# Performance work log

Measured on AMD Instinct MI355X. Metric: run time of the kernel, lower is better.

## Reference

```python
import jax, jax.numpy as jnp
import numpy as np

N_NODES = 50000
N_GRAPHS = 256
IN_DIM = 128
HID = 128
N_LAYERS = 3
N_EDGES = 800000


def setup_inputs() -> dict:
    key = jax.random.key(0)
    ks = jax.random.split(key, 16)
    x = jax.random.normal(ks[0], (N_NODES, IN_DIM), dtype=jnp.float32)
    edge_index = jax.random.randint(ks[1], (2, N_EDGES), 0, N_NODES, dtype=jnp.int64)
    batch = jnp.sort(jax.random.randint(ks[2], (N_NODES,), 0, N_GRAPHS, dtype=jnp.int64))
    inp = {"x": x, "edge_index": edge_index, "batch": batch}
    # SAGEConv params per PyG: lin_l (bias) applied to mean-aggregated neighbors,
    # lin_r (no bias) applied to the root node feature.
    dims = [(IN_DIM, HID)] + [(HID, HID)] * (N_LAYERS - 1)
    for i, (din, dout) in enumerate(dims):
        s = 1.0 / np.sqrt(din)
        inp[f"Wl{i}"] = jax.random.uniform(ks[3 + 3 * i], (din, dout), jnp.float32, -s, s)
        inp[f"bl{i}"] = jax.random.uniform(ks[4 + 3 * i], (dout,), jnp.float32, -s, s)
        inp[f"Wr{i}"] = jax.random.uniform(ks[5 + 3 * i], (din, dout), jnp.float32, -s, s)
    return inp


def _sage_conv(x, src, dst, Wl, bl, Wr):
    # mean aggregation of source-node messages into destination nodes
    msg = x[src]                                               # [E, d] gather
    agg = jax.ops.segment_sum(msg, dst, num_segments=N_NODES)  # [N, d] scatter-add
    deg = jax.ops.segment_sum(jnp.ones((src.shape[0], 1), x.dtype), dst,
                              num_segments=N_NODES)
    agg = agg / jnp.maximum(deg, 1.0)
    return agg @ Wl + bl + x @ Wr


def reference(x, edge_index, batch, Wl0, bl0, Wr0, Wl1, bl1, Wr1, Wl2, bl2, Wr2):
    src, dst = edge_index[0], edge_index[1]
    params = [(Wl0, bl0, Wr0), (Wl1, bl1, Wr1), (Wl2, bl2, Wr2)]
    h = x
    for Wl, bl, Wr in params:
        h = jax.nn.relu(_sage_conv(h, src, dst, Wl, bl, Wr))
        # dropout is a no-op in eval mode
    # meanmax readout over graph ids
    cnt = jax.ops.segment_sum(jnp.ones((h.shape[0], 1), h.dtype), batch,
                              num_segments=N_GRAPHS)
    g_mean = jax.ops.segment_sum(h, batch, num_segments=N_GRAPHS) / jnp.maximum(cnt, 1.0)
    g_max = jax.ops.segment_max(h, batch, num_segments=N_GRAPHS)
    g_max = jnp.where(jnp.isfinite(g_max), g_max, 0.0)  # empty graphs -> 0
    return jnp.concatenate([g_mean, g_max], axis=-1)    # [G, 2*HID]
```

## Files before the change

kernel.cpp:

```cpp
#include <hip/hip_runtime.h>
#include <hip/hip_bf16.h>
#include <stdint.h>

#define N_NODES  50000
#define N_GRAPHS 256
#define DIM      128
#define N_EDGES  800000
#define K2       256
#define N_STRIPS (N_NODES / 16)
#define PAD_CAP  64

typedef __attribute__((ext_vector_type(8))) short  short8;
typedef __attribute__((ext_vector_type(4))) float  floatx4;
typedef __attribute__((ext_vector_type(4))) int    intx4;

__device__ __forceinline__ ushort f2bf(float f) {
    union { float f; uint32_t u; } c; c.f = f;
    uint32_t u = c.u;
    return (ushort)((u + 0x7fffu + ((u >> 16) & 1u)) >> 16);
}

#define MB_CONV 6250
#define MB_PREPW (MB_CONV + 384)
#define MB_GB   (MB_PREPW + 196)
#define MB_CNT  (MB_GB + 196)
#define MB_OUT  (MB_CNT + 256)
__global__ __launch_bounds__(256) void k_misc(const float* __restrict__ x, ushort* __restrict__ xb,
                                              const float* __restrict__ Wl0, const float* __restrict__ Wr0,
                                              const float* __restrict__ Wl1, const float* __restrict__ Wr1,
                                              const float* __restrict__ Wl2, const float* __restrict__ Wr2,
                                              ushort* __restrict__ Wt,
                                              const int* __restrict__ batch,
                                              int* __restrict__ gstart, int* __restrict__ gend,
                                              int* __restrict__ cnt, float* __restrict__ out) {
    int b = blockIdx.x, t = threadIdx.x;
    if (b < MB_CONV) {
        int i = b * 256 + t;
        float4 v = ((const float4*)x)[i];
        uint32_t lo = (uint32_t)f2bf(v.x) | ((uint32_t)f2bf(v.y) << 16);
        uint32_t hi = (uint32_t)f2bf(v.z) | ((uint32_t)f2bf(v.w) << 16);
        ((uint2*)xb)[i] = make_uint2(lo, hi);
    } else if (b < MB_PREPW) {
        int i = (b - MB_CONV) * 256 + t;
        int layer = i / (DIM * K2);
        int j = i % (DIM * K2);
        int n = j / K2, k = j % K2;
        const float* Wl = (layer == 0) ? Wl0 : (layer == 1) ? Wl1 : Wl2;
        const float* Wr = (layer == 0) ? Wr0 : (layer == 1) ? Wr1 : Wr2;
        float v = (k < DIM) ? Wl[k * DIM + n] : Wr[(k - DIM) * DIM + n];
        Wt[i] = f2bf(v);
    } else if (b < MB_GB) {
        int i = (b - MB_PREPW) * 256 + t;
        if (i < N_NODES) {
            int g = batch[i];
            if (i == 0) gstart[g] = 0;
            int gn = (i + 1 < N_NODES) ? batch[i + 1] : -1;
            if (gn != g) {
                gend[g] = i + 1;
                if (gn >= 0) gstart[gn] = i + 1;
            }
        }
    } else if (b < MB_CNT) {
        int i = (b - MB_GB) * 256 + t;
        if (i < N_NODES) cnt[i] = 0;
    } else {
        int i = (b - MB_CNT) * 256 + t;
        if (i < N_GRAPHS * 2 * DIM) out[i] = 0.f;
    }
}

__global__ __launch_bounds__(256) void k_build_direct(const int* __restrict__ src,
                                                      const int* __restrict__ dst,
                                                      int* __restrict__ cnt,
                                                      int* __restrict__ padded) {
    int i = blockIdx.x * 256 + threadIdx.x;
    if (i < N_EDGES) {
        int d = dst[i], s = src[i];
        int p = atomicAdd(&cnt[d], 1);
        if (p < PAD_CAP) padded[(size_t)d * PAD_CAP + p] = s;
    }
}

template <int MODE>
__global__ __launch_bounds__(256) void k_layer(const ushort* __restrict__ h_in,
                                               int* __restrict__ padded,
                                               const int* __restrict__ cnt,
                                               const ushort* __restrict__ Wt,
                                               const float* __restrict__ bias,
                                               ushort* __restrict__ out_bf,
                                               const int* __restrict__ batch,
                                               float* __restrict__ gout) {
    __shared__ ushort sAgg[16 * DIM];
    __shared__ int    sIdx[16 * PAD_CAP];
    __shared__ int    sCnt[16];
    __shared__ int    sChl[4][17];
    __shared__ int    sNch[4];
    __shared__ int    sGb[(MODE == 2) ? 16 : 1];
    __shared__ float  hTile[(MODE == 2) ? 16 * DIM : 1];

    int t    = threadIdx.x;
    int wid  = t >> 6;
    int lane = t & 63;
    int r0   = blockIdx.x * 16;
    const uint32_t* hw = (const uint32_t*)h_in;

    ((intx4*)sIdx)[t] = __builtin_nontemporal_load(
        ((const intx4*)(padded + (size_t)r0 * PAD_CAP)) + t);
    if (t < 16) sCnt[t] = cnt[r0 + t];
    if (MODE == 2 && t >= 16 && t < 32) sGb[t - 16] = batch[r0 + t - 16];
    __syncthreads();

    if (MODE == 0) {
        #pragma unroll
        for (int q = 0; q < 4; ++q) {
            int nl  = wid * 4 + q;
            int m   = min(sCnt[nl], PAD_CAP);
            int* lst = sIdx + nl * PAD_CAP;
            int v = (lane < m) ? lst[lane] : 0x7fffffff;
            #pragma unroll
            for (int k = 2; k <= 64; k <<= 1) {
                #pragma unroll
                for (int j = k >> 1; j > 0; j >>= 1) {
                    int other  = __shfl_xor(v, j, 64);
                    bool down  = (lane & k) != 0;
                    bool lower = (lane & j) == 0;
                    v = (lower ^ down) ? min(v, other) : max(v, other);
                }
            }
            if (lane < m) {
                lst[lane] = v;
                __builtin_nontemporal_store(v,
                    &padded[(size_t)(r0 + nl) * PAD_CAP + lane]);
            }
        }
    }

    if (lane == 0) {
        int n = 0;
        #pragma unroll
        for (int q = 0; q < 4; ++q) {
            int m = min(sCnt[wid * 4 + q], PAD_CAP);
            for (int e0 = 0; e0 < m; e0 += 16)
                sChl[wid][n++] = q | (e0 << 8);
        }
        sNch[wid] = n;
    }
    #pragma unroll
    for (int q = 0; q < 4; ++q) {
        int node = wid * 4 + q;
        if (sCnt[node] == 0) ((uint32_t*)(sAgg + node * DIM))[lane] = 0u;
    }
    int nch = sNch[wid];

    float ax[4] = {0.f, 0.f, 0.f, 0.f};
    float ay[4] = {0.f, 0.f, 0.f, 0.f};
    uint32_t va[16], vb[16];

    auto issue = [&](int ci, uint32_t (&v)[16]) {
        int ch   = sChl[wid][ci];
        int q    = ch & 255, e0 = ch >> 8;
        int node = wid * 4 + q;
        int m    = min(sCnt[node], PAD_CAP);
        const int* lst = sIdx + node * PAD_CAP;
        #pragma unroll
        for (int k = 0; k < 16; ++k) {
            int ek = e0 + k;
            int id = lst[ek < m ? ek : m - 1];
            v[k] = hw[(size_t)id * 64 + lane];
        }
    };
    auto consume = [&](int ci, uint32_t (&v)[16], bool isLast) {
        int ch   = sChl[wid][ci];
        int q    = ch & 255, e0 = ch >> 8;
        int node = wid * 4 + q;
        int deg  = sCnt[node];
        int m    = min(deg, PAD_CAP);
        #pragma unroll
        for (int k = 0; k < 16; ++k) {
            uint32_t w = (e0 + k < m) ? v[k] : 0u;
            ax[k & 3] += __uint_as_float(w << 16);
            ay[k & 3] += __uint_as_float(w & 0xffff0000u);
        }
        bool lastOfNode = isLast || ((sChl[wid][ci + 1] & 255) != q);
        if (lastOfNode) {
            float axs = (ax[0] + ax[1]) + (ax[2] + ax[3]);
            float ays = (ay[0] + ay[1]) + (ay[2] + ay[3]);
            float inv = 1.0f / (float)(deg > 0 ? deg : 1);
            uint32_t o = (uint32_t)f2bf(axs * inv) | ((uint32_t)f2bf(ays * inv) << 16);
            ((uint32_t*)(sAgg + node * DIM))[lane] = o;
            #pragma unroll
            for (int j = 0; j < 4; ++j) { ax[j] = 0.f; ay[j] = 0.f; }
        }
    };

    if (nch > 0) {
        issue(0, va);
        int i = 0;
        while (true) {
            bool hasB = (i + 1) < nch;
            if (hasB) issue(i + 1, vb);
            consume(i, va, !hasB);
            if (!hasB) break;
            bool hasA = (i + 2) < nch;
            if (hasA) issue(i + 2, va);
            consume(i + 1, vb, !hasA);
            if (!hasA) break;
            i += 2;
        }
    }
    __syncthreads();

    int row  = lane & 15;
    int quad = lane >> 4;
    short8 a[8];
    const ushort* srow = sAgg + row * DIM + quad * 8;
    #pragma unroll
    for (int ks = 0; ks < 4; ++ks) a[ks] = *(const short8*)(srow + ks * 32);
    const ushort* hrow = h_in + (size_t)(r0 + row) * DIM + quad * 8;
    #pragma unroll
    for (int ks = 0; ks < 4; ++ks) a[4 + ks] = *(const short8*)(hrow + ks * 32);

    #pragma unroll
    for (int c = 0; c < 2; ++c) {
        int ct  = wid * 2 + c;
        int col = ct * 16 + row;
        const ushort* wrow = Wt + (size_t)col * K2 + quad * 8;
        floatx4 acc = {0.f, 0.f, 0.f, 0.f};
        #pragma unroll
        for (int ks = 0; ks < 8; ++ks) {
            short8 b = *(const short8*)(wrow + ks * 32);
            acc = __builtin_amdgcn_mfma_f32_16x16x32_bf16(a[ks], b, acc, 0, 0, 0);
        }
        float bv = bias[col];
        #pragma unroll
        for (int r = 0; r < 4; ++r) {
            int m = r0 + quad * 4 + r;
            float v = acc[r] + bv;
            v = v > 0.f ? v : 0.f;
            if (MODE < 2) __builtin_nontemporal_store(f2bf(v), &out_bf[(size_t)m * DIM + col]);
            else          hTile[(quad * 4 + r) * DIM + col] = v;
        }
    }

    if (MODE == 2) {
        __syncthreads();
        int d     = t & 127;
        bool doMax = t >= 128;
        float s = 0.f, mx = 0.f;
        int cur = sGb[0];
        #pragma unroll
        for (int m = 0; m < 16; ++m) {
            int g = sGb[m];
            if (g != cur) {
                if (doMax) atomicMax((int*)&gout[cur * 2 * DIM + DIM + d], __float_as_int(mx));
                else       atomicAdd(&gout[cur * 2 * DIM + d], s);
                cur = g; s = 0.f; mx = 0.f;
            }
            float v = hTile[m * DIM + d];
            s += v; mx = fmaxf(mx, v);
        }
        if (doMax) atomicMax((int*)&gout[cur * 2 * DIM + DIM + d], __float_as_int(mx));
        else       atomicAdd(&gout[cur * 2 * DIM + d], s);
    }
}

__global__ __launch_bounds__(256) void k_finalize(float* __restrict__ out,
                                                  const int* __restrict__ gstart,
                                                  const int* __restrict__ gend) {
    int i = blockIdx.x * 256 + threadIdx.x;
    if (i < N_GRAPHS * DIM) {
        int g = i / DIM, d = i % DIM;
        int c = gend[g] - gstart[g];
        out[g * 2 * DIM + d] /= (float)(c > 0 ? c : 1);
    }
}

extern "C" void kernel_launch(void* const* d_in, const int* in_sizes, int n_in,
                              void* d_out, int out_size, void* d_ws, size_t ws_size,
                              hipStream_t stream) {
    const float* x     = (const float*)d_in[0];
    const int*   ei    = (const int*)d_in[1];
    const int*   src   = ei;
    const int*   dst   = ei + N_EDGES;
    const int*   batch = (const int*)d_in[2];
    const float* Wl[3] = {(const float*)d_in[3], (const float*)d_in[6], (const float*)d_in[9]};
    const float* bl[3] = {(const float*)d_in[4], (const float*)d_in[7], (const float*)d_in[10]};
    const float* Wr[3] = {(const float*)d_in[5], (const float*)d_in[8], (const float*)d_in[11]};
    float* out = (float*)d_out;

    char* base = (char*)d_ws;
    size_t o = 0;
    auto alloc = [&](size_t b) -> char* {
        char* p = base + o;
        o = (o + b + 255) & ~(size_t)255;
        return p;
    };
    int*     gstart = (int*)alloc((size_t)N_GRAPHS * 4);
    int*     gend   = (int*)alloc((size_t)N_GRAPHS * 4);
    int*     cnt    = (int*)alloc((size_t)N_NODES * 4);
    int*     padded = (int*)alloc((size_t)N_NODES * PAD_CAP * 4);
    ushort*  xb     = (ushort*)alloc((size_t)N_NODES * DIM * 2);
    ushort*  ha     = (ushort*)alloc((size_t)N_NODES * DIM * 2);
    ushort*  hb     = (ushort*)alloc((size_t)N_NODES * DIM * 2);
    ushort*  Wt     = (ushort*)alloc((size_t)3 * DIM * K2 * 2);
    (void)ws_size; (void)n_in; (void)in_sizes; (void)out_size;

    k_misc<<<MB_OUT, 256, 0, stream>>>(x, xb, Wl[0], Wr[0], Wl[1], Wr[1], Wl[2], Wr[2],
                                       Wt, batch, gstart, gend, cnt, out);
    k_build_direct<<<(N_EDGES + 255) / 256, 256, 0, stream>>>(src, dst, cnt, padded);

    k_layer<0><<<N_STRIPS, 256, 0, stream>>>(xb, padded, cnt, Wt,                bl[0], ha, batch, out);
    k_layer<1><<<N_STRIPS, 256, 0, stream>>>(ha, padded, cnt, Wt + DIM * K2,     bl[1], hb, batch, out);
    k_layer<2><<<N_STRIPS, 256, 0, stream>>>(hb, padded, cnt, Wt + 2 * DIM * K2, bl[2], nullptr, batch, out);

    k_finalize<<<(N_GRAPHS * DIM + 255) / 256, 256, 0, stream>>>(out, gstart, gend);
}
```

Measured before the change: 327.4 us.

## Give each wave its own 16-node strip and drop block barriers in layer kernel

Each wavefront now handles a whole 16-node strip on its own: it loads the strip's neighbour lists, sorts and gathers them, and runs all 8 MFMA column tiles. Blocks therefore carry four independent strips and need no __syncthreads. The aggregation buffer reuses the index shared memory. The final-layer readout now reduces sum and max per graph segment with cross-lane shuffles and issues fewer atomics, instead of staging a shared tile. The edge-build scatter uses nontemporal stores. In exchange, each wave does more serial work and holds more registers, and the grid has a quarter as many blocks.

```diff
diff --git a/kernel.cpp b/kernel.cpp
--- a/kernel.cpp
+++ b/kernel.cpp
@@ -77,7 +77,7 @@
     if (i < N_EDGES) {
         int d = dst[i], s = src[i];
         int p = atomicAdd(&cnt[d], 1);
-        if (p < PAD_CAP) padded[(size_t)d * PAD_CAP + p] = s;
+        if (p < PAD_CAP) __builtin_nontemporal_store(s, &padded[(size_t)d * PAD_CAP + p]);
     }
 }
 
@@ -90,32 +90,32 @@
                                                ushort* __restrict__ out_bf,
                                                const int* __restrict__ batch,
                                                float* __restrict__ gout) {
-    __shared__ ushort sAgg[16 * DIM];
-    __shared__ int    sIdx[16 * PAD_CAP];
-    __shared__ int    sCnt[16];
-    __shared__ int    sChl[4][17];
-    __shared__ int    sNch[4];
-    __shared__ int    sGb[(MODE == 2) ? 16 : 1];
-    __shared__ float  hTile[(MODE == 2) ? 16 * DIM : 1];
-
-    int t    = threadIdx.x;
-    int wid  = t >> 6;
-    int lane = t & 63;
-    int r0   = blockIdx.x * 16;
+    __shared__ int sIA[4][16 * 64];
+    __shared__ int sCnt[4][16];
+    __shared__ int sChl[4][65];
+    __shared__ int sGb[4][16];
+
+    int t     = threadIdx.x;
+    int wid   = t >> 6;
+    int lane  = t & 63;
+    int strip = blockIdx.x * 4 + wid;
+    if (strip >= N_STRIPS) return;
+    int r0    = strip * 16;
+    int* sIdx = sIA[wid];
     const uint32_t* hw = (const uint32_t*)h_in;
 
-    ((intx4*)sIdx)[t] = __builtin_nontemporal_load(
-        ((const intx4*)(padded + (size_t)r0 * PAD_CAP)) + t);
-    if (t < 16) sCnt[t] = cnt[r0 + t];
-    if (MODE == 2 && t >= 16 && t < 32) sGb[t - 16] = batch[r0 + t - 16];
-    __syncthreads();
+    const intx4* gsrc = (const intx4*)(padded + (size_t)r0 * PAD_CAP);
+    #pragma unroll
+    for (int it = 0; it < 4; ++it)
+        ((intx4*)sIdx)[it * 64 + lane] = __builtin_nontemporal_load(gsrc + it * 64 + lane);
+    if (lane < 16) sCnt[wid][lane] = cnt[r0 + lane];
+    if (MODE == 2 && lane >= 16 && lane < 32) sGb[wid][lane - 16] = batch[r0 + lane - 16];
 
     if (MODE == 0) {
-        #pragma unroll
-        for (int q = 0; q < 4; ++q) {
-            int nl  = wid * 4 + q;
-            int m   = min(sCnt[nl], PAD_CAP);
-            int* lst = sIdx + nl * PAD_CAP;
+        #pragma unroll 1
+        for (int q = 0; q < 16; ++q) {
+            int m = min(sCnt[wid][q], PAD_CAP);
+            int* lst = sIdx + q * 64;
             int v = (lane < m) ? lst[lane] : 0x7fffffff;
             #pragma unroll
             for (int k = 2; k <= 64; k <<= 1) {
@@ -130,38 +130,35 @@
             if (lane < m) {
                 lst[lane] = v;
                 __builtin_nontemporal_store(v,
-                    &padded[(size_t)(r0 + nl) * PAD_CAP + lane]);
+                    &padded[(size_t)(r0 + q) * PAD_CAP + lane]);
             }
         }
     }
 
     if (lane == 0) {
         int n = 0;
-        #pragma unroll
-        for (int q = 0; q < 4; ++q) {
-            int m = min(sCnt[wid * 4 + q], PAD_CAP);
+        #pragma unroll 1
+        for (int q = 0; q < 16; ++q) {
+            int m = min(sCnt[wid][q], PAD_CAP);
             for (int e0 = 0; e0 < m; e0 += 16)
                 sChl[wid][n++] = q | (e0 << 8);
         }
-        sNch[wid] = n;
-    }
-    #pragma unroll
-    for (int q = 0; q < 4; ++q) {
-        int node = wid * 4 + q;
-        if (sCnt[node] == 0) ((uint32_t*)(sAgg + node * DIM))[lane] = 0u;
-    }
-    int nch = sNch[wid];
+        sChl[wid][64] = n;
+    }
+    #pragma unroll 1
+    for (int q = 0; q < 16; ++q)
+        if (sCnt[wid][q] == 0) ((uint32_t*)(sIdx + q * 64))[lane] = 0u;
+    int nch = sChl[wid][64];
 
     float ax[4] = {0.f, 0.f, 0.f, 0.f};
     float ay[4] = {0.f, 0.f, 0.f, 0.f};
     uint32_t va[16], vb[16];
 
     auto issue = [&](int ci, uint32_t (&v)[16]) {
-        int ch   = sChl[wid][ci];
-        int q    = ch & 255, e0 = ch >> 8;
-        int node = wid * 4 + q;
-        int m    = min(sCnt[node], PAD_CAP);
-        const int* lst = sIdx + node * PAD_CAP;
+        int ch = sChl[wid][ci];
+        int q  = ch & 255, e0 = ch >> 8;
+        int m  = min(sCnt[wid][q], PAD_CAP);
+        const int* lst = sIdx + q * 64;
         #pragma unroll
         for (int k = 0; k < 16; ++k) {
             int ek = e0 + k;
@@ -170,11 +167,10 @@
         }
     };
     auto consume = [&](int ci, uint32_t (&v)[16], bool isLast) {
-        int ch   = sChl[wid][ci];
-        int q    = ch & 255, e0 = ch >> 8;
-        int node = wid * 4 + q;
-        int deg  = sCnt[node];
-        int m    = min(deg, PAD_CAP);
+        int ch  = sChl[wid][ci];
+        int q   = ch & 255, e0 = ch >> 8;
+        int deg = sCnt[wid][q];
+        int m   = min(deg, PAD_CAP);
         #pragma unroll
         for (int k = 0; k < 16; ++k) {
             uint32_t w = (e0 + k < m) ? v[k] : 0u;
@@ -187,7 +183,7 @@
             float ays = (ay[0] + ay[1]) + (ay[2] + ay[3]);
             float inv = 1.0f / (float)(deg > 0 ? deg : 1);
             uint32_t o = (uint32_t)f2bf(axs * inv) | ((uint32_t)f2bf(ays * inv) << 16);
-            ((uint32_t*)(sAgg + node * DIM))[lane] = o;
+            ((uint32_t*)(sIdx + q * 64))[lane] = o;
             #pragma unroll
             for (int j = 0; j < 4; ++j) { ax[j] = 0.f; ay[j] = 0.f; }
         }
@@ -208,21 +204,19 @@
             i += 2;
         }
     }
-    __syncthreads();
 
     int row  = lane & 15;
     int quad = lane >> 4;
     short8 a[8];
-    const ushort* srow = sAgg + row * DIM + quad * 8;
+    const ushort* srow = (const ushort*)sIdx + row * 128 + quad * 8;
     #pragma unroll
     for (int ks = 0; ks < 4; ++ks) a[ks] = *(const short8*)(srow + ks * 32);
     const ushort* hrow = h_in + (size_t)(r0 + row) * DIM + quad * 8;
     #pragma unroll
     for (int ks = 0; ks < 4; ++ks) a[4 + ks] = *(const short8*)(hrow + ks * 32);
 
-    #pragma unroll
-    for (int c = 0; c < 2; ++c) {
-        int ct  = wid * 2 + c;
+    #pragma unroll 1
+    for (int ct = 0; ct < 8; ++ct) {
         int col = ct * 16 + row;
         const ushort* wrow = Wt + (size_t)col * K2 + quad * 8;
         floatx4 acc = {0.f, 0.f, 0.f, 0.f};
@@ -232,35 +226,42 @@
             acc = __builtin_amdgcn_mfma_f32_16x16x32_bf16(a[ks], b, acc, 0, 0, 0);
         }
         float bv = bias[col];
+        float v[4];
         #pragma unroll
         for (int r = 0; r < 4; ++r) {
-            int m = r0 + quad * 4 + r;
-            float v = acc[r] + bv;
-            v = v > 0.f ? v : 0.f;
-            if (MODE < 2) __builtin_nontemporal_store(f2bf(v), &out_bf[(size_t)m * DIM + col]);
-            else          hTile[(quad * 4 + r) * DIM + col] = v;
-        }
-    }
-
-    if (MODE == 2) {
-        __syncthreads();
-        int d     = t & 127;
-        bool doMax = t >= 128;
-        float s = 0.f, mx = 0.f;
-        int cur = sGb[0];
-        #pragma unroll
-        for (int m = 0; m < 16; ++m) {
-            int g = sGb[m];
-            if (g != cur) {
-                if (doMax) atomicMax((int*)&gout[cur * 2 * DIM + DIM + d], __float_as_int(mx));
-                else       atomicAdd(&gout[cur * 2 * DIM + d], s);
-                cur = g; s = 0.f; mx = 0.f;
+            float u = acc[r] + bv;
+            v[r] = u > 0.f ? u : 0.f;
+        }
+        if (MODE < 2) {
+            #pragma unroll
+            for (int r = 0; r < 4; ++r)
+                __builtin_nontemporal_store(f2bf(v[r]),
+                    &out_bf[(size_t)(r0 + quad * 4 + r) * DIM + col]);
+        } else {
+            int s0 = 0;
+            while (s0 < 16) {
+                int g  = sGb[wid][s0];
+                int s1 = s0 + 1;
+                while (s1 < 16 && sGb[wid][s1] == g) ++s1;
+                float sm = 0.f, mx = 0.f;
+                #pragma unroll
+                for (int r = 0; r < 4; ++r) {
+                    int rr = quad * 4 + r;
+                    bool in = (rr >= s0) && (rr < s1);
+                    sm += in ? v[r] : 0.f;
+                    mx = fmaxf(mx, in ? v[r] : 0.f);
+                }
+                sm += __shfl_xor(sm, 16, 64);
+                sm += __shfl_xor(sm, 32, 64);
+                mx = fmaxf(mx, __shfl_xor(mx, 16, 64));
+                mx = fmaxf(mx, __shfl_xor(mx, 32, 64));
+                if (quad == 0) {
+                    atomicAdd(&gout[g * 2 * DIM + col], sm);
+                    atomicMax((int*)&gout[g * 2 * DIM + DIM + col], __float_as_int(mx));
+                }
+                s0 = s1;
             }
-            float v = hTile[m * DIM + d];
-            s += v; mx = fmaxf(mx, v);
-        }
-        if (doMax) atomicMax((int*)&gout[cur * 2 * DIM + DIM + d], __float_as_int(mx));
-        else       atomicAdd(&gout[cur * 2 * DIM + d], s);
+        }
     }
 }
 
@@ -305,13 +306,15 @@
     ushort*  Wt     = (ushort*)alloc((size_t)3 * DIM * K2 * 2);
     (void)ws_size; (void)n_in; (void)in_sizes; (void)out_size;
 
+    const int LGRID = (N_STRIPS + 3) / 4;
+
     k_misc<<<MB_OUT, 256, 0, stream>>>(x, xb, Wl[0], Wr[0], Wl[1], Wr[1], Wl[2], Wr[2],
                                        Wt, batch, gstart, gend, cnt, out);
     k_build_direct<<<(N_EDGES + 255) / 256, 256, 0, stream>>>(src, dst, cnt, padded);
 
-    k_layer<0><<<N_STRIPS, 256, 0, stream>>>(xb, padded, cnt, Wt,                bl[0], ha, batch, out);
-    k_layer<1><<<N_STRIPS, 256, 0, stream>>>(ha, padded, cnt, Wt + DIM * K2,     bl[1], hb, batch, out);
-    k_layer<2><<<N_STRIPS, 256, 0, stream>>>(hb, padded, cnt, Wt + 2 * DIM * K2, bl[2], nullptr, batch, out);
+    k_layer<0><<<LGRID, 256, 0, stream>>>(xb, padded, cnt, Wt,                bl[0], ha, batch, out);
+    k_layer<1><<<LGRID, 256, 0, stream>>>(ha, padded, cnt, Wt + DIM * K2,     bl[1], hb, batch, out);
+    k_layer<2><<<LGRID, 256, 0, stream>>>(hb, padded, cnt, Wt + 2 * DIM * K2, bl[2], nullptr, batch, out);
 
     k_finalize<<<(N_GRAPHS * DIM + 255) / 256, 256, 0, stream>>>(out, gstart, gend);
 }
```

Measured after the change: 367.7 us. 12.3% more time.

## Reorder neighbor gather chunks by source-node range to improve cache locality

Applied to the files above, without the earlier changes.

Splits each node's sorted neighbor list into four source-ID ranges and schedules gather chunks pass by pass across the wave's four nodes, so concurrent loads touch a narrower region of the feature table. Partial sums are accumulated in a shared float2 buffer instead of registers, and that buffer is reused as the readout tile. The build kernel also writes the padded adjacency with nontemporal stores. This adds more, smaller chunks and extra LDS read-modify-writes per chunk in exchange for better L2 locality.

```diff
diff --git a/kernel.cpp b/kernel.cpp
--- a/kernel.cpp
+++ b/kernel.cpp
@@ -9,6 +9,8 @@
 #define K2       256
 #define N_STRIPS (N_NODES / 16)
 #define PAD_CAP  64
+#define NPASS    4
+#define RANGE    12500
 
 typedef __attribute__((ext_vector_type(8))) short  short8;
 typedef __attribute__((ext_vector_type(4))) float  floatx4;
@@ -77,7 +79,7 @@
     if (i < N_EDGES) {
         int d = dst[i], s = src[i];
         int p = atomicAdd(&cnt[d], 1);
-        if (p < PAD_CAP) padded[(size_t)d * PAD_CAP + p] = s;
+        if (p < PAD_CAP) __builtin_nontemporal_store(s, &padded[(size_t)d * PAD_CAP + p]);
     }
 }
 
@@ -92,11 +94,10 @@
                                                float* __restrict__ gout) {
     __shared__ ushort sAgg[16 * DIM];
     __shared__ int    sIdx[16 * PAD_CAP];
+    __shared__ float2 sAcc[16 * 64];
     __shared__ int    sCnt[16];
-    __shared__ int    sChl[4][17];
-    __shared__ int    sNch[4];
+    __shared__ int    sChl[4][28];
     __shared__ int    sGb[(MODE == 2) ? 16 : 1];
-    __shared__ float  hTile[(MODE == 2) ? 16 * DIM : 1];
 
     int t    = threadIdx.x;
     int wid  = t >> 6;
@@ -108,6 +109,9 @@
         ((const intx4*)(padded + (size_t)r0 * PAD_CAP)) + t);
     if (t < 16) sCnt[t] = cnt[r0 + t];
     if (MODE == 2 && t >= 16 && t < 32) sGb[t - 16] = batch[r0 + t - 16];
+    #pragma unroll
+    for (int q = 0; q < 4; ++q)
+        sAcc[(wid * 4 + q) * 64 + lane] = make_float2(0.f, 0.f);
     __syncthreads();
 
     if (MODE == 0) {
@@ -135,62 +139,60 @@
         }
     }
 
-    if (lane == 0) {
-        int n = 0;
-        #pragma unroll
-        for (int q = 0; q < 4; ++q) {
-            int m = min(sCnt[wid * 4 + q], PAD_CAP);
-            for (int e0 = 0; e0 < m; e0 += 16)
-                sChl[wid][n++] = q | (e0 << 8);
-        }
-        sNch[wid] = n;
-    }
+    int ee[4][NPASS + 1];
     #pragma unroll
     for (int q = 0; q < 4; ++q) {
         int node = wid * 4 + q;
-        if (sCnt[node] == 0) ((uint32_t*)(sAgg + node * DIM))[lane] = 0u;
-    }
-    int nch = sNch[wid];
-
-    float ax[4] = {0.f, 0.f, 0.f, 0.f};
-    float ay[4] = {0.f, 0.f, 0.f, 0.f};
+        int m = min(sCnt[node], PAD_CAP);
+        int vq = (lane < m) ? sIdx[node * PAD_CAP + lane] : 0x7fffffff;
+        ee[q][0] = 0;
+        ee[q][NPASS] = m;
+        #pragma unroll
+        for (int p = 1; p < NPASS; ++p)
+            ee[q][p] = (int)__popcll(__ballot(vq < p * RANGE));
+    }
+    int nch = 0;
+    #pragma unroll
+    for (int p = 0; p < NPASS; ++p) {
+        #pragma unroll
+        for (int q = 0; q < 4; ++q) {
+            int e0 = ee[q][p], e1 = ee[q][p + 1];
+            for (; e0 < e1; e0 += 16) {
+                if (lane == 0) sChl[wid][nch] = q | (e0 << 8) | (e1 << 16);
+                ++nch;
+            }
+        }
+    }
+
     uint32_t va[16], vb[16];
 
     auto issue = [&](int ci, uint32_t (&v)[16]) {
-        int ch   = sChl[wid][ci];
-        int q    = ch & 255, e0 = ch >> 8;
+        int ch  = sChl[wid][ci];
+        int q   = ch & 15, e0 = (ch >> 8) & 255, end = ch >> 16;
         int node = wid * 4 + q;
-        int m    = min(sCnt[node], PAD_CAP);
         const int* lst = sIdx + node * PAD_CAP;
         #pragma unroll
         for (int k = 0; k < 16; ++k) {
             int ek = e0 + k;
-            int id = lst[ek < m ? ek : m - 1];
+            int id = lst[ek < end ? ek : end - 1];
             v[k] = hw[(size_t)id * 64 + lane];
         }
     };
-    auto consume = [&](int ci, uint32_t (&v)[16], bool isLast) {
-        int ch   = sChl[wid][ci];
-        int q    = ch & 255, e0 = ch >> 8;
+    auto consume = [&](int ci, uint32_t (&v)[16]) {
+        int ch  = sChl[wid][ci];
+        int q   = ch & 15, e0 = (ch >> 8) & 255, end = ch >> 16;
         int node = wid * 4 + q;
-        int deg  = sCnt[node];
-        int m    = min(deg, PAD_CAP);
+        float ax0 = 0.f, ax1 = 0.f, ay0 = 0.f, ay1 = 0.f;
         #pragma unroll
         for (int k = 0; k < 16; ++k) {
-            uint32_t w = (e0 + k < m) ? v[k] : 0u;
-            ax[k & 3] += __uint_as_float(w << 16);
-            ay[k & 3] += __uint_as_float(w & 0xffff0000u);
-        }
-        bool lastOfNode = isLast || ((sChl[wid][ci + 1] & 255) != q);
-        if (lastOfNode) {
-            float axs = (ax[0] + ax[1]) + (ax[2] + ax[3]);
-            float ays = (ay[0] + ay[1]) + (ay[2] + ay[3]);
-            float inv = 1.0f / (float)(deg > 0 ? deg : 1);
-            uint32_t o = (uint32_t)f2bf(axs * inv) | ((uint32_t)f2bf(ays * inv) << 16);
-            ((uint32_t*)(sAgg + node * DIM))[lane] = o;
-            #pragma unroll
-            for (int j = 0; j < 4; ++j) { ax[j] = 0.f; ay[j] = 0.f; }
-        }
+            uint32_t w = (e0 + k < end) ? v[k] : 0u;
+            if (k & 1) { ax1 += __uint_as_float(w << 16); ay1 += __uint_as_float(w & 0xffff0000u); }
+            else       { ax0 += __uint_as_float(w << 16); ay0 += __uint_as_float(w & 0xffff0000u); }
+        }
+        float2* acc = &sAcc[node * 64 + lane];
+        float2 c = *acc;
+        c.x += ax0 + ax1; c.y += ay0 + ay1;
+        *acc = c;
     };
 
     if (nch > 0) {
@@ -199,17 +201,27 @@
         while (true) {
             bool hasB = (i + 1) < nch;
             if (hasB) issue(i + 1, vb);
-            consume(i, va, !hasB);
+            consume(i, va);
             if (!hasB) break;
             bool hasA = (i + 2) < nch;
             if (hasA) issue(i + 2, va);
-            consume(i + 1, vb, !hasA);
+            consume(i + 1, vb);
             if (!hasA) break;
             i += 2;
         }
     }
+    #pragma unroll
+    for (int q = 0; q < 4; ++q) {
+        int node = wid * 4 + q;
+        int deg  = sCnt[node];
+        float inv = 1.0f / (float)(deg > 0 ? deg : 1);
+        float2 c = sAcc[node * 64 + lane];
+        uint32_t o = (uint32_t)f2bf(c.x * inv) | ((uint32_t)f2bf(c.y * inv) << 16);
+        ((uint32_t*)(sAgg + node * DIM))[lane] = o;
+    }
     __syncthreads();
 
+    float* hTile = (float*)sAcc;
     int row  = lane & 15;
     int quad = lane >> 4;
     short8 a[8];
```

Measured after the change: 442.6 us. +35.2%, slower.
